# Kernel tuning notes

Hardware: AMD Instinct MI355X
Metric: run time of the kernel (lower is better)

The kernel has to match this reference:

```python
import jax, jax.numpy as jnp
import numpy as np

EMBED = 1024
HEADS = 16
HEAD_DIM = EMBED // HEADS


def setup_inputs() -> dict:
    key = jax.random.key(0)
    ks = jax.random.split(key, 9)
    s = 1.0 / np.sqrt(EMBED)
    x = jax.random.normal(ks[0], (2, 2048, EMBED), dtype=jnp.float32)
    Wq = jax.random.uniform(ks[1], (EMBED, EMBED), jnp.float32, -s, s)
    bq = jax.random.uniform(ks[2], (EMBED,), jnp.float32, -s, s)
    Wk = jax.random.uniform(ks[3], (EMBED, EMBED), jnp.float32, -s, s)
    bk = jax.random.uniform(ks[4], (EMBED,), jnp.float32, -s, s)
    Wv = jax.random.uniform(ks[5], (EMBED, EMBED), jnp.float32, -s, s)
    bv = jax.random.uniform(ks[6], (EMBED,), jnp.float32, -s, s)
    Wo = jax.random.uniform(ks[7], (EMBED, EMBED), jnp.float32, -s, s)
    bo = jax.random.uniform(ks[8], (EMBED,), jnp.float32, -s, s)
    return {"x": x, "Wq": Wq, "bq": bq, "Wk": Wk, "bk": bk,
            "Wv": Wv, "bv": bv, "Wo": Wo, "bo": bo}


def reference(x, Wq, bq, Wk, bk, Wv, bv, Wo, bo):
    B, S, E = x.shape
    H, D = HEADS, HEAD_DIM
    # QKV projections, split heads: [B,S,E] -> [B,H,S,D]
    def proj(W, b):
        return (x @ W + b).reshape(B, S, H, D).transpose(0, 2, 1, 3)
    q, k, v = proj(Wq, bq), proj(Wk, bk), proj(Wv, bv)
    scores = jnp.einsum('bhsd,bhtd->bhst', q, k) / jnp.sqrt(jnp.float32(D))
    attn = jax.nn.softmax(scores, axis=-1)
    out = jnp.einsum('bhst,bhtd->bhsd', attn, v)  # [B,H,S,D]
    out = out.transpose(0, 2, 1, 3).reshape(B, S, E)
    return out @ Wo + bo
```

## Files before the change

kernel.cpp:

```cpp
#include <hip/hip_runtime.h>
#include <cstddef>
#include <cstdint>

#define EMB 1024
#define NH 16
#define HD 64
#define SEQ 2048
#define BATCH 2
#define MROWS 4096
#define LOG2E 1.4426950408889634f

typedef unsigned short u16;
typedef __attribute__((ext_vector_type(8))) short short8;
typedef __attribute__((ext_vector_type(4))) short short4v;
typedef __attribute__((ext_vector_type(4))) float floatx4;

#define MFMA32(a,b,c) __builtin_amdgcn_mfma_f32_16x16x32_bf16((a),(b),(c),0,0,0)

#if __has_builtin(__builtin_amdgcn_mfma_f32_16x16x16bf16_1k)
#define PVMFMA(a,b,c) __builtin_amdgcn_mfma_f32_16x16x16bf16_1k((a),(b),(c),0,0,0)
#elif __has_builtin(__builtin_amdgcn_mfma_f32_16x16x16_bf16)
#define PVMFMA(a,b,c) __builtin_amdgcn_mfma_f32_16x16x16_bf16((a),(b),(c),0,0,0)
#else
__device__ __forceinline__ floatx4 pv_mfma_fb(short4v a, short4v b, floatx4 c) {
    short8 a8 = {a.x, a.y, a.z, a.w, 0, 0, 0, 0};
    short8 b8 = {b.x, b.y, b.z, b.w, 0, 0, 0, 0};
    return MFMA32(a8, b8, c);
}
#define PVMFMA(a,b,c) pv_mfma_fb((a),(b),(c))
#endif

__device__ __forceinline__ u16 f2bf(float f) {
    union { float f; uint32_t u; } v; v.f = f;
    return (u16)((v.u + 0x7fffu + ((v.u >> 16) & 1u)) >> 16);
}
__device__ __forceinline__ uint32_t pk_trunc(float a, float b) {
    union { float f; uint32_t u; } va, vb; va.f = a; vb.f = b;
    return __builtin_amdgcn_perm(vb.u, va.u, 0x07060302u);
}
__device__ __forceinline__ float lo_f(uint32_t u) {
    union { uint32_t u; float f; } v; v.u = u << 16; return v.f;
}
__device__ __forceinline__ float hi_f(uint32_t u) {
    union { uint32_t u; float f; } v; v.u = u & 0xffff0000u; return v.f;
}
typedef const __attribute__((address_space(1))) void* gptr_t;
typedef __attribute__((address_space(3))) void* lptr_t;
__device__ __forceinline__ void gl2lds16(const void* g, void* l) {
    __builtin_amdgcn_global_load_lds((gptr_t)g, (lptr_t)l, 16, 0, 0);
}

__global__ __launch_bounds__(256) void cvt_x_k(const float* __restrict__ x,
                                               u16* __restrict__ xh) {
    const int stride = gridDim.x * 256 * 8;
    for (int i = (blockIdx.x * 256 + threadIdx.x) * 8; i < MROWS * EMB; i += stride) {
        float4 a = *(const float4*)(x + i);
        float4 b = *(const float4*)(x + i + 4);
        alignas(16) u16 o[8] = {f2bf(a.x), f2bf(a.y), f2bf(a.z), f2bf(a.w),
                                f2bf(b.x), f2bf(b.y), f2bf(b.z), f2bf(b.w)};
        *(uint4*)(xh + i) = *(const uint4*)o;
    }
}

__global__ __launch_bounds__(256) void cvt_wt_k(
    const float* __restrict__ W0, const float* __restrict__ W1,
    const float* __restrict__ W2, const float* __restrict__ W3,
    u16* __restrict__ Wt4) {
    const int z = blockIdx.z;
    const float* W = (z == 0) ? W0 : (z == 1) ? W1 : (z == 2) ? W2 : W3;
    const float scale = (z == 0) ? 0.125f * LOG2E : 1.0f;
    u16* dst = Wt4 + (size_t)z * 1048576;
    __shared__ float Lf[64][65];
    const int kt = blockIdx.y * 64, nt = blockIdx.x * 64;
    const int tid = threadIdx.x;
    {
        const int r = tid >> 2, c4 = (tid & 3) * 16;
        const float* src = W + (size_t)(kt + r) * EMB + nt + c4;
        #pragma unroll
        for (int i = 0; i < 16; i += 4) {
            float4 v = *(const float4*)(src + i);
            Lf[r][c4 + i + 0] = v.x; Lf[r][c4 + i + 1] = v.y;
            Lf[r][c4 + i + 2] = v.z; Lf[r][c4 + i + 3] = v.w;
        }
    }
    __syncthreads();
    const int n = tid >> 2, k4 = (tid & 3) * 16;
    alignas(16) u16 hb[16];
    #pragma unroll
    for (int i = 0; i < 16; ++i) hb[i] = f2bf(Lf[k4 + i][n] * scale);
    const size_t o = (size_t)(nt + n) * EMB + kt + k4;
    *(uint4*)(dst + o) = *(const uint4*)hb;
    *(uint4*)(dst + o + 8) = *(const uint4*)(hb + 8);
}

__global__ __launch_bounds__(256) void gemm_qkv_k(
    const u16* __restrict__ xh, const u16* __restrict__ Wt4,
    const float* __restrict__ b0, const float* __restrict__ b1,
    const float* __restrict__ b2,
    u16* __restrict__ Q, u16* __restrict__ K, u16* __restrict__ V) {
    const int z = blockIdx.z;
    const u16* Wt = Wt4 + (size_t)z * 1048576;
    const float* bias = (z == 0) ? b0 : (z == 1) ? b1 : b2;
    u16* out = (z == 0) ? Q : (z == 1) ? K : V;
    const float bscale = (z == 0) ? 0.125f * LOG2E : 1.0f;
    const int bm = blockIdx.y * 128, bn = blockIdx.x * 128;
    __shared__ alignas(16) u16 As[4096];
    __shared__ alignas(16) u16 Bs[4096];
    const int tid = threadIdx.x;
    const int lane = tid & 63, w = tid >> 6;
    const int l15 = lane & 15, quad = lane >> 4;
    const int wm = (w & 1) * 64, wn = (w >> 1) * 64;

    floatx4 acc[4][4];
    const floatx4 zf = {0.f, 0.f, 0.f, 0.f};
    #pragma unroll
    for (int mt = 0; mt < 4; ++mt)
        #pragma unroll
        for (int nt = 0; nt < 4; ++nt) acc[mt][nt] = zf;

    const int c0 = tid, c1 = tid + 256;
    const int r0 = c0 >> 2, p0 = c0 & 3, cc0 = (p0 - r0 - (r0 >> 2)) & 3;
    const int r1 = c1 >> 2, p1 = c1 & 3, cc1 = (p1 - r1 - (r1 >> 2)) & 3;
    const u16* ag0 = xh + (size_t)(bm + r0) * EMB + cc0 * 8;
    const u16* ag1 = xh + (size_t)(bm + r1) * EMB + cc1 * 8;
    const u16* bg0 = Wt + (size_t)(bn + r0) * EMB + cc0 * 8;
    const u16* bg1 = Wt + (size_t)(bn + r1) * EMB + cc1 * 8;

    for (int kt = 0; kt < EMB; kt += 32) {
        __syncthreads();
        gl2lds16(ag0 + kt, &As[c0 * 8]); gl2lds16(ag1 + kt, &As[c1 * 8]);
        gl2lds16(bg0 + kt, &Bs[c0 * 8]); gl2lds16(bg1 + kt, &Bs[c1 * 8]);
        __syncthreads();
        short8 af[4], bf[4];
        #pragma unroll
        for (int t = 0; t < 4; ++t) {
            const int ra = wm + t * 16 + l15;
            const int rb = wn + t * 16 + l15;
            af[t] = *(const short8*)&As[ra * 32 + ((quad + ra + (ra >> 2)) & 3) * 8];
            bf[t] = *(const short8*)&Bs[rb * 32 + ((quad + rb + (rb >> 2)) & 3) * 8];
        }
        #pragma unroll
        for (int mt = 0; mt < 4; ++mt)
            #pragma unroll
            for (int nt = 0; nt < 4; ++nt)
                acc[mt][nt] = MFMA32(af[mt], bf[nt], acc[mt][nt]);
    }

    #pragma unroll
    for (int nt = 0; nt < 4; ++nt) {
        const int col = bn + wn + nt * 16 + l15;
        const float bv = bias[col] * bscale;
        #pragma unroll
        for (int mt = 0; mt < 4; ++mt) {
            const int row = bm + wm + mt * 16 + quad * 4;
            #pragma unroll
            for (int r = 0; r < 4; ++r)
                out[(size_t)(row + r) * EMB + col] = f2bf(acc[mt][nt][r] + bv);
        }
    }
}

__global__ __launch_bounds__(256) void gemm_o_k(
    const u16* __restrict__ Ag, const u16* __restrict__ Wt,
    const float* __restrict__ bias, float* __restrict__ out) {
    const int bm = blockIdx.y * 128, bn = blockIdx.x * 64;
    __shared__ alignas(16) u16 As[4096];
    __shared__ alignas(16) u16 Bs[2048];
    const int tid = threadIdx.x;
    const int lane = tid & 63, w = tid >> 6;
    const int l15 = lane & 15, quad = lane >> 4;
    const int wm = w * 32;

    floatx4 acc[2][4];
    const floatx4 zf = {0.f, 0.f, 0.f, 0.f};
    #pragma unroll
    for (int mt = 0; mt < 2; ++mt)
        #pragma unroll
        for (int nt = 0; nt < 4; ++nt) acc[mt][nt] = zf;

    const int c0 = tid, c1 = tid + 256;
    const int r0 = c0 >> 2, p0 = c0 & 3, cc0 = (p0 - r0 - (r0 >> 2)) & 3;
    const int r1 = c1 >> 2, p1 = c1 & 3, cc1 = (p1 - r1 - (r1 >> 2)) & 3;
    const u16* ag0 = Ag + (size_t)(bm + r0) * EMB + cc0 * 8;
    const u16* ag1 = Ag + (size_t)(bm + r1) * EMB + cc1 * 8;
    const u16* bg0 = Wt + (size_t)(bn + r0) * EMB + cc0 * 8;

    for (int kt = 0; kt < EMB; kt += 32) {
        __syncthreads();
        gl2lds16(ag0 + kt, &As[c0 * 8]);
        gl2lds16(ag1 + kt, &As[c1 * 8]);
        if (c0 < 256) gl2lds16(bg0 + kt, &Bs[c0 * 8]);
        __syncthreads();
        short8 af[2], bf[4];
        #pragma unroll
        for (int t = 0; t < 2; ++t) {
            const int ra = wm + t * 16 + l15;
            af[t] = *(const short8*)&As[ra * 32 + ((quad + ra + (ra >> 2)) & 3) * 8];
        }
        #pragma unroll
        for (int t = 0; t < 4; ++t) {
            const int rb = t * 16 + l15;
            bf[t] = *(const short8*)&Bs[rb * 32 + ((quad + rb + (rb >> 2)) & 3) * 8];
        }
        #pragma unroll
        for (int mt = 0; mt < 2; ++mt)
            #pragma unroll
            for (int nt = 0; nt < 4; ++nt)
                acc[mt][nt] = MFMA32(af[mt], bf[nt], acc[mt][nt]);
    }

    #pragma unroll
    for (int nt = 0; nt < 4; ++nt) {
        const int col = bn + nt * 16 + l15;
        const float bv = bias[col];
        #pragma unroll
        for (int mt = 0; mt < 2; ++mt) {
            const int row = bm + wm + mt * 16 + quad * 4;
            #pragma unroll
            for (int r = 0; r < 4; ++r)
                out[(size_t)(row + r) * EMB + col] = acc[mt][nt][r] + bv;
        }
    }
}

__global__ __launch_bounds__(256) void vtrans_k(const u16* __restrict__ V,
                                                u16* __restrict__ Vt) {
    const int tt = blockIdx.x, h = blockIdx.y, b = blockIdx.z;
    __shared__ u16 Lt[64][72];
    const int tid = threadIdx.x;
    {
        const int r = tid >> 2, c4 = (tid & 3) * 16;
        const u16* src = V + (size_t)(b * SEQ + tt * 64 + r) * EMB + h * HD + c4;
        alignas(16) u16 buf[16];
        *(uint4*)buf = *(const uint4*)src;
        *(uint4*)(buf + 8) = *(const uint4*)(src + 8);
        #pragma unroll
        for (int i = 0; i < 16; ++i) Lt[c4 + i][r] = buf[i];
    }
    __syncthreads();
    const int d = tid >> 2, t4 = (tid & 3) * 16;
    u16* dst = Vt + ((size_t)((b * NH + h) * HD + d)) * SEQ + tt * 64 + t4;
    *(uint4*)dst = *(const uint4*)&Lt[d][t4];
    *(uint4*)(dst + 8) = *(const uint4*)&Lt[d][t4 + 8];
}

__global__ __launch_bounds__(256) void flash_k(
    const u16* __restrict__ Q, const u16* __restrict__ K,
    const u16* __restrict__ Vt, u16* __restrict__ Np0, u16* __restrict__ Np1,
    float* __restrict__ Lp) {
    const int qt = blockIdx.x, h = blockIdx.y;
    const int b = blockIdx.z >> 1, half = blockIdx.z & 1;
    const int t0 = half * (SEQ / 2);
    __shared__ alignas(16) u16 Ks[4096];
    __shared__ alignas(16) u16 Vs[4096];
    const int tid = threadIdx.x;
    const int lane = tid & 63, w = tid >> 6;
    const int l15 = lane & 15, quad = lane >> 4;

    const u16* qp = Q + (size_t)(b * SEQ + qt * 128 + w * 32 + l15) * EMB + h * HD + quad * 8;
    short8 qb[2][2];
    qb[0][0] = *(const short8*)qp;
    qb[0][1] = *(const short8*)(qp + 32);
    qb[1][0] = *(const short8*)(qp + 16 * EMB);
    qb[1][1] = *(const short8*)(qp + 16 * EMB + 32);

    const floatx4 zf = {0.f, 0.f, 0.f, 0.f};
    floatx4 oacc[2][4];
    float l_part[2] = {0.f, 0.f};
    #pragma unroll
    for (int u = 0; u < 2; ++u)
        #pragma unroll
        for (int nt = 0; nt < 4; ++nt) oacc[u][nt] = zf;

    const int s0 = tid, s1 = tid + 256;
    const int kr0 = s0 >> 3, kc0 = ((s0 & 7) - kr0) & 7;
    const int kr1 = s1 >> 3, kc1 = ((s1 & 7) - kr1) & 7;
    const u16* kg0 = K + (size_t)(b * SEQ + t0 + kr0) * EMB + h * HD + kc0 * 8;
    const u16* kg1 = K + (size_t)(b * SEQ + t0 + kr1) * EMB + h * HD + kc1 * 8;
    const u16* vg0 = Vt + ((size_t)((b * NH + h) * HD + kr0)) * SEQ + t0 + kc0 * 8;
    const u16* vg1 = Vt + ((size_t)((b * NH + h) * HD + kr1)) * SEQ + t0 + kc1 * 8;

    for (int kt = 0; kt < SEQ / 2 / 64; ++kt) {
        __syncthreads();
        gl2lds16(kg0 + (size_t)kt * 64 * EMB, &Ks[s0 * 8]);
        gl2lds16(kg1 + (size_t)kt * 64 * EMB, &Ks[s1 * 8]);
        gl2lds16(vg0 + kt * 64, &Vs[s0 * 8]);
        gl2lds16(vg1 + kt * 64, &Vs[s1 * 8]);
        __syncthreads();

        floatx4 sa[2][4];
        #pragma unroll
        for (int mt = 0; mt < 4; ++mt) {
            const int r = mt * 16 + l15;
            const short8 ka0 = *(const short8*)&Ks[r * 64 + ((quad + r) & 7) * 8];
            const short8 ka1 = *(const short8*)&Ks[r * 64 + ((quad + 4 + r) & 7) * 8];
            #pragma unroll
            for (int u = 0; u < 2; ++u)
                sa[u][mt] = MFMA32(ka1, qb[u][1], MFMA32(ka0, qb[u][0], zf));
        }

        short4v pfr[2][4];
        #pragma unroll
        for (int u = 0; u < 2; ++u)
            #pragma unroll
            for (int mt = 0; mt < 4; ++mt) {
                const float e0 = exp2f(sa[u][mt][0]);
                const float e1 = exp2f(sa[u][mt][1]);
                const float e2 = exp2f(sa[u][mt][2]);
                const float e3 = exp2f(sa[u][mt][3]);
                const uint32_t u01 = pk_trunc(e0, e1);
                const uint32_t u23 = pk_trunc(e2, e3);
                l_part[u] += (lo_f(u01) + hi_f(u01)) + (lo_f(u23) + hi_f(u23));
                union { uint32_t uu[2]; short4v s; } pk;
                pk.uu[0] = u01; pk.uu[1] = u23;
                pfr[u][mt] = pk.s;
            }

        #pragma unroll
        for (int mt = 0; mt < 4; ++mt) {
            const int c16 = mt * 2 + (quad >> 1);
            const int hof = (quad & 1) * 4;
            #pragma unroll
            for (int nt = 0; nt < 4; ++nt) {
                const int vr = nt * 16 + l15;
                const short4v vb =
                    *(const short4v*)&Vs[vr * 64 + ((c16 + vr) & 7) * 8 + hof];
                #pragma unroll
                for (int u = 0; u < 2; ++u)
                    oacc[u][nt] = PVMFMA(pfr[u][mt], vb, oacc[u][nt]);
            }
        }
    }

    u16* np = half ? Np1 : Np0;
    float* lp = Lp + (size_t)half * (MROWS * NH);

    #pragma unroll
    for (int u = 0; u < 2; ++u) {
        l_part[u] += __shfl_xor(l_part[u], 16, 64);
        l_part[u] += __shfl_xor(l_part[u], 32, 64);
        if (quad == 0) {
            const int qrow = qt * 128 + w * 32 + u * 16 + l15;
            lp[(size_t)(b * SEQ + qrow) * NH + h] = l_part[u];
        }
    }

    #pragma unroll
    for (int u = 0; u < 2; ++u)
        #pragma unroll
        for (int r = 0; r < 4; ++r) {
            const size_t o =
                (size_t)(b * SEQ + qt * 128 + w * 32 + u * 16 + quad * 4 + r) * EMB
                + h * HD + l15;
            #pragma unroll
            for (int nt = 0; nt < 4; ++nt)
                np[o + nt * 16] = f2bf(oacc[u][nt][r]);
        }
}

__global__ __launch_bounds__(256) void reduce_k(
    const u16* __restrict__ Np0, const u16* __restrict__ Np1,
    const float* __restrict__ Lp, u16* __restrict__ AO) {
    const int i = blockIdx.x * 256 + threadIdx.x;
    const int e = i * 4;
    const int row = e >> 10;
    const int hh = (e & 1023) >> 6;
    const float inv =
        1.f / (Lp[(size_t)row * NH + hh] + Lp[(size_t)MROWS * NH + (size_t)row * NH + hh]);
    const uint2 n0 = *(const uint2*)(Np0 + e);
    const uint2 n1 = *(const uint2*)(Np1 + e);
    const float x0 = (lo_f(n0.x) + lo_f(n1.x)) * inv;
    const float x1 = (hi_f(n0.x) + hi_f(n1.x)) * inv;
    const float x2 = (lo_f(n0.y) + lo_f(n1.y)) * inv;
    const float x3 = (hi_f(n0.y) + hi_f(n1.y)) * inv;
    uint2 o;
    o.x = (uint32_t)f2bf(x0) | ((uint32_t)f2bf(x1) << 16);
    o.y = (uint32_t)f2bf(x2) | ((uint32_t)f2bf(x3) << 16);
    *(uint2*)(AO + e) = o;
}

extern "C" void kernel_launch(void* const* d_in, const int* in_sizes, int n_in,
                              void* d_out, int out_size, void* d_ws, size_t ws_size,
                              hipStream_t stream) {
    const float* x  = (const float*)d_in[0];
    const float* Wq = (const float*)d_in[1];
    const float* bq = (const float*)d_in[2];
    const float* Wk = (const float*)d_in[3];
    const float* bk = (const float*)d_in[4];
    const float* Wv = (const float*)d_in[5];
    const float* bv = (const float*)d_in[6];
    const float* Wo = (const float*)d_in[7];
    const float* bo = (const float*)d_in[8];

    u16* ws16 = (u16*)d_ws;
    const size_t P4 = (size_t)MROWS * EMB;
    u16* xh  = ws16;
    u16* Qb  = ws16 + P4;
    u16* Kb  = ws16 + 2 * P4;
    u16* Vb  = ws16 + 3 * P4;
    u16* Vtb = ws16 + 4 * P4;
    u16* Wt4 = ws16 + 5 * P4;
    float* Lp = (float*)(ws16 + 6 * P4);

    cvt_x_k<<<1024, 256, 0, stream>>>(x, xh);
    cvt_wt_k<<<dim3(16, 16, 4), 256, 0, stream>>>(Wq, Wk, Wv, Wo, Wt4);
    gemm_qkv_k<<<dim3(8, 32, 3), 256, 0, stream>>>(xh, Wt4, bq, bk, bv, Qb, Kb, Vb);
    vtrans_k<<<dim3(32, 16, 2), 256, 0, stream>>>(Vb, Vtb);
    flash_k<<<dim3(16, 16, 4), 256, 0, stream>>>(Qb, Kb, Vtb, xh, Vb, Lp);
    reduce_k<<<4096, 256, 0, stream>>>(xh, Vb, Lp, Qb);
    gemm_o_k<<<dim3(16, 32, 1), 256, 0, stream>>>(Qb, Wt4 + 3 * 1048576, bo, (float*)d_out);
}
```

Baseline: 222.8 us.

## Fuse conversions, write V transposed from QKV GEMM, split flash KV four ways

Merges the x and weight conversion kernels into one launch and removes the separate V-transpose kernel. The QKV GEMM now writes V straight into the transposed [b,h,d,t] layout using 8-byte stores. Flash attention splits the key range four ways instead of two, doubling the grid for more parallelism, and the reduce kernel combines four partials. In exchange there is extra workspace, more partial traffic in the reduce step, and scattered strided stores for V.

```diff
diff --git a/kernel.cpp b/kernel.cpp
--- a/kernel.cpp
+++ b/kernel.cpp
@@ -50,29 +50,31 @@
     __builtin_amdgcn_global_load_lds((gptr_t)g, (lptr_t)l, 16, 0, 0);
 }
 
-__global__ __launch_bounds__(256) void cvt_x_k(const float* __restrict__ x,
-                                               u16* __restrict__ xh) {
-    const int stride = gridDim.x * 256 * 8;
-    for (int i = (blockIdx.x * 256 + threadIdx.x) * 8; i < MROWS * EMB; i += stride) {
-        float4 a = *(const float4*)(x + i);
-        float4 b = *(const float4*)(x + i + 4);
-        alignas(16) u16 o[8] = {f2bf(a.x), f2bf(a.y), f2bf(a.z), f2bf(a.w),
-                                f2bf(b.x), f2bf(b.y), f2bf(b.z), f2bf(b.w)};
-        *(uint4*)(xh + i) = *(const uint4*)o;
-    }
-}
-
-__global__ __launch_bounds__(256) void cvt_wt_k(
+__global__ __launch_bounds__(256) void cvt_all_k(
+    const float* __restrict__ x,
     const float* __restrict__ W0, const float* __restrict__ W1,
     const float* __restrict__ W2, const float* __restrict__ W3,
-    u16* __restrict__ Wt4) {
+    u16* __restrict__ Wt4, u16* __restrict__ xh) {
     const int z = blockIdx.z;
+    const int tid = threadIdx.x;
+    if (z == 4) {
+        const int nb = gridDim.x * gridDim.y;
+        const int bid = blockIdx.y * gridDim.x + blockIdx.x;
+        const int stride = nb * 256 * 8;
+        for (int i = (bid * 256 + tid) * 8; i < MROWS * EMB; i += stride) {
+            float4 a = *(const float4*)(x + i);
+            float4 b = *(const float4*)(x + i + 4);
+            alignas(16) u16 o[8] = {f2bf(a.x), f2bf(a.y), f2bf(a.z), f2bf(a.w),
+                                    f2bf(b.x), f2bf(b.y), f2bf(b.z), f2bf(b.w)};
+            *(uint4*)(xh + i) = *(const uint4*)o;
+        }
+        return;
+    }
     const float* W = (z == 0) ? W0 : (z == 1) ? W1 : (z == 2) ? W2 : W3;
     const float scale = (z == 0) ? 0.125f * LOG2E : 1.0f;
     u16* dst = Wt4 + (size_t)z * 1048576;
     __shared__ float Lf[64][65];
     const int kt = blockIdx.y * 64, nt = blockIdx.x * 64;
-    const int tid = threadIdx.x;
     {
         const int r = tid >> 2, c4 = (tid & 3) * 16;
         const float* src = W + (size_t)(kt + r) * EMB + nt + c4;
@@ -97,11 +99,10 @@
     const u16* __restrict__ xh, const u16* __restrict__ Wt4,
     const float* __restrict__ b0, const float* __restrict__ b1,
     const float* __restrict__ b2,
-    u16* __restrict__ Q, u16* __restrict__ K, u16* __restrict__ V) {
+    u16* __restrict__ Q, u16* __restrict__ K, u16* __restrict__ Vt) {
     const int z = blockIdx.z;
     const u16* Wt = Wt4 + (size_t)z * 1048576;
     const float* bias = (z == 0) ? b0 : (z == 1) ? b1 : b2;
-    u16* out = (z == 0) ? Q : (z == 1) ? K : V;
     const float bscale = (z == 0) ? 0.125f * LOG2E : 1.0f;
     const int bm = blockIdx.y * 128, bn = blockIdx.x * 128;
     __shared__ alignas(16) u16 As[4096];
@@ -146,16 +147,36 @@
                 acc[mt][nt] = MFMA32(af[mt], bf[nt], acc[mt][nt]);
     }
 
-    #pragma unroll
-    for (int nt = 0; nt < 4; ++nt) {
-        const int col = bn + wn + nt * 16 + l15;
-        const float bv = bias[col] * bscale;
-        #pragma unroll
-        for (int mt = 0; mt < 4; ++mt) {
-            const int row = bm + wm + mt * 16 + quad * 4;
-            #pragma unroll
-            for (int r = 0; r < 4; ++r)
-                out[(size_t)(row + r) * EMB + col] = f2bf(acc[mt][nt][r] + bv);
+    if (z != 2) {
+        u16* out = (z == 0) ? Q : K;
+        #pragma unroll
+        for (int nt = 0; nt < 4; ++nt) {
+            const int col = bn + wn + nt * 16 + l15;
+            const float bv = bias[col] * bscale;
+            #pragma unroll
+            for (int mt = 0; mt < 4; ++mt) {
+                const int row = bm + wm + mt * 16 + quad * 4;
+                #pragma unroll
+                for (int r = 0; r < 4; ++r)
+                    out[(size_t)(row + r) * EMB + col] = f2bf(acc[mt][nt][r] + bv);
+            }
+        }
+    } else {
+        #pragma unroll
+        for (int nt = 0; nt < 4; ++nt) {
+            const int col = bn + wn + nt * 16 + l15;
+            const int hh = col >> 6, d = col & 63;
+            const float bv = bias[col];
+            #pragma unroll
+            for (int mt = 0; mt < 4; ++mt) {
+                const int row = bm + wm + mt * 16 + quad * 4;
+                const int bb = row >> 11, t0 = row & 2047;
+                alignas(8) u16 pk4[4];
+                #pragma unroll
+                for (int r = 0; r < 4; ++r) pk4[r] = f2bf(acc[mt][nt][r] + bv);
+                *(uint2*)(Vt + ((size_t)((bb * NH + hh) * HD + d)) * SEQ + t0) =
+                    *(const uint2*)pk4;
+            }
         }
     }
 }
@@ -223,34 +244,15 @@
     }
 }
 
-__global__ __launch_bounds__(256) void vtrans_k(const u16* __restrict__ V,
-                                                u16* __restrict__ Vt) {
-    const int tt = blockIdx.x, h = blockIdx.y, b = blockIdx.z;
-    __shared__ u16 Lt[64][72];
-    const int tid = threadIdx.x;
-    {
-        const int r = tid >> 2, c4 = (tid & 3) * 16;
-        const u16* src = V + (size_t)(b * SEQ + tt * 64 + r) * EMB + h * HD + c4;
-        alignas(16) u16 buf[16];
-        *(uint4*)buf = *(const uint4*)src;
-        *(uint4*)(buf + 8) = *(const uint4*)(src + 8);
-        #pragma unroll
-        for (int i = 0; i < 16; ++i) Lt[c4 + i][r] = buf[i];
-    }
-    __syncthreads();
-    const int d = tid >> 2, t4 = (tid & 3) * 16;
-    u16* dst = Vt + ((size_t)((b * NH + h) * HD + d)) * SEQ + tt * 64 + t4;
-    *(uint4*)dst = *(const uint4*)&Lt[d][t4];
-    *(uint4*)(dst + 8) = *(const uint4*)&Lt[d][t4 + 8];
-}
-
 __global__ __launch_bounds__(256) void flash_k(
     const u16* __restrict__ Q, const u16* __restrict__ K,
-    const u16* __restrict__ Vt, u16* __restrict__ Np0, u16* __restrict__ Np1,
+    const u16* __restrict__ Vt,
+    u16* __restrict__ Np0, u16* __restrict__ Np1,
+    u16* __restrict__ Np2, u16* __restrict__ Np3,
     float* __restrict__ Lp) {
     const int qt = blockIdx.x, h = blockIdx.y;
-    const int b = blockIdx.z >> 1, half = blockIdx.z & 1;
-    const int t0 = half * (SEQ / 2);
+    const int b = blockIdx.z >> 2, sp = blockIdx.z & 3;
+    const int t0 = sp * (SEQ / 4);
     __shared__ alignas(16) u16 Ks[4096];
     __shared__ alignas(16) u16 Vs[4096];
     const int tid = threadIdx.x;
@@ -280,7 +282,7 @@
     const u16* vg0 = Vt + ((size_t)((b * NH + h) * HD + kr0)) * SEQ + t0 + kc0 * 8;
     const u16* vg1 = Vt + ((size_t)((b * NH + h) * HD + kr1)) * SEQ + t0 + kc1 * 8;
 
-    for (int kt = 0; kt < SEQ / 2 / 64; ++kt) {
+    for (int kt = 0; kt < SEQ / 4 / 64; ++kt) {
         __syncthreads();
         gl2lds16(kg0 + (size_t)kt * 64 * EMB, &Ks[s0 * 8]);
         gl2lds16(kg1 + (size_t)kt * 64 * EMB, &Ks[s1 * 8]);
@@ -332,8 +334,8 @@
         }
     }
 
-    u16* np = half ? Np1 : Np0;
-    float* lp = Lp + (size_t)half * (MROWS * NH);
+    u16* np = (sp == 0) ? Np0 : (sp == 1) ? Np1 : (sp == 2) ? Np2 : Np3;
+    float* lp = Lp + (size_t)sp * (MROWS * NH);
 
     #pragma unroll
     for (int u = 0; u < 2; ++u) {
@@ -360,19 +362,25 @@
 
 __global__ __launch_bounds__(256) void reduce_k(
     const u16* __restrict__ Np0, const u16* __restrict__ Np1,
+    const u16* __restrict__ Np2, const u16* __restrict__ Np3,
     const float* __restrict__ Lp, u16* __restrict__ AO) {
     const int i = blockIdx.x * 256 + threadIdx.x;
     const int e = i * 4;
     const int row = e >> 10;
     const int hh = (e & 1023) >> 6;
-    const float inv =
-        1.f / (Lp[(size_t)row * NH + hh] + Lp[(size_t)MROWS * NH + (size_t)row * NH + hh]);
+    const size_t lx = (size_t)row * NH + hh;
+    const float lsum = Lp[lx] + Lp[(size_t)(MROWS * NH) + lx] +
+                       Lp[2 * (size_t)(MROWS * NH) + lx] +
+                       Lp[3 * (size_t)(MROWS * NH) + lx];
+    const float inv = 1.f / lsum;
     const uint2 n0 = *(const uint2*)(Np0 + e);
     const uint2 n1 = *(const uint2*)(Np1 + e);
-    const float x0 = (lo_f(n0.x) + lo_f(n1.x)) * inv;
-    const float x1 = (hi_f(n0.x) + hi_f(n1.x)) * inv;
-    const float x2 = (lo_f(n0.y) + lo_f(n1.y)) * inv;
-    const float x3 = (hi_f(n0.y) + hi_f(n1.y)) * inv;
+    const uint2 n2 = *(const uint2*)(Np2 + e);
+    const uint2 n3 = *(const uint2*)(Np3 + e);
+    const float x0 = (lo_f(n0.x) + lo_f(n1.x) + lo_f(n2.x) + lo_f(n3.x)) * inv;
+    const float x1 = (hi_f(n0.x) + hi_f(n1.x) + hi_f(n2.x) + hi_f(n3.x)) * inv;
+    const float x2 = (lo_f(n0.y) + lo_f(n1.y) + lo_f(n2.y) + lo_f(n3.y)) * inv;
+    const float x3 = (hi_f(n0.y) + hi_f(n1.y) + hi_f(n2.y) + hi_f(n3.y)) * inv;
     uint2 o;
     o.x = (uint32_t)f2bf(x0) | ((uint32_t)f2bf(x1) << 16);
     o.y = (uint32_t)f2bf(x2) | ((uint32_t)f2bf(x3) << 16);
@@ -397,16 +405,16 @@
     u16* xh  = ws16;
     u16* Qb  = ws16 + P4;
     u16* Kb  = ws16 + 2 * P4;
-    u16* Vb  = ws16 + 3 * P4;
-    u16* Vtb = ws16 + 4 * P4;
-    u16* Wt4 = ws16 + 5 * P4;
-    float* Lp = (float*)(ws16 + 6 * P4);
-
-    cvt_x_k<<<1024, 256, 0, stream>>>(x, xh);
-    cvt_wt_k<<<dim3(16, 16, 4), 256, 0, stream>>>(Wq, Wk, Wv, Wo, Wt4);
-    gemm_qkv_k<<<dim3(8, 32, 3), 256, 0, stream>>>(xh, Wt4, bq, bk, bv, Qb, Kb, Vb);
-    vtrans_k<<<dim3(32, 16, 2), 256, 0, stream>>>(Vb, Vtb);
-    flash_k<<<dim3(16, 16, 4), 256, 0, stream>>>(Qb, Kb, Vtb, xh, Vb, Lp);
-    reduce_k<<<4096, 256, 0, stream>>>(xh, Vb, Lp, Qb);
+    u16* Vtb = ws16 + 3 * P4;
+    u16* Wt4 = ws16 + 4 * P4;
+    u16* N1  = ws16 + 5 * P4;
+    u16* N2  = ws16 + 6 * P4;
+    u16* N3  = ws16 + 7 * P4;
+    float* Lp = (float*)(ws16 + 8 * P4);
+
+    cvt_all_k<<<dim3(16, 16, 5), 256, 0, stream>>>(x, Wq, Wk, Wv, Wo, Wt4, xh);
+    gemm_qkv_k<<<dim3(8, 32, 3), 256, 0, stream>>>(xh, Wt4, bq, bk, bv, Qb, Kb, Vtb);
+    flash_k<<<dim3(16, 16, 8), 256, 0, stream>>>(Qb, Kb, Vtb, xh, N1, N2, N3, Lp);
+    reduce_k<<<4096, 256, 0, stream>>>(xh, N1, N2, N3, Lp, Qb);
     gemm_o_k<<<dim3(16, 32, 1), 256, 0, stream>>>(Qb, Wt4 + 3 * 1048576, bo, (float*)d_out);
 }
```

Measured after the change: 235.4 us. 5.7% more time.
